# Performance work log

Measured on AMD Instinct MI355X. Metric: run time of the kernel, lower is better.

## Reference

```python
import jax, jax.numpy as jnp
import numpy as np

P = 262144
H = 256
EPS = 1e-12  # torch F.normalize eps


def _l2norm(x):
    # matches torch.nn.functional.normalize(x, dim=-1): x / max(||x||, eps)
    n = jnp.linalg.norm(x, axis=-1, keepdims=True)
    return x / jnp.maximum(n, EPS)


def _mlp(x, params):
    # params: list of (W, b); ReLU on all but last layer
    for W, b in params[:-1]:
        x = jax.nn.relu(x @ W + b)
    W, b = params[-1]
    return x @ W + b


def setup_inputs() -> dict:
    key = jax.random.key(0)
    ks = jax.random.split(key, 24)
    inp = {
        "normals": jax.random.normal(ks[0], (P, 3), dtype=jnp.float32),
        "view_dirs": jax.random.normal(ks[1], (P, 3), dtype=jnp.float32),
        "roughness": jax.random.uniform(ks[2], (P, 1), dtype=jnp.float32),
        "r0": jax.random.uniform(ks[3], (P, 1), dtype=jnp.float32),
    }
    # diffuse MLP: 3 -> 256 -> 256 -> 256 -> 3
    d_dims = [3, H, H, H, 3]
    # specular MLP: 8 -> 256 -> 256 -> 256 -> 3
    s_dims = [8, H, H, H, 3]
    k = 4
    for i in range(4):
        fan = d_dims[i]
        inp[f"dW{i}"] = jax.random.normal(ks[k], (d_dims[i], d_dims[i + 1]), dtype=jnp.float32) * (2.0 / fan) ** 0.5
        inp[f"db{i}"] = jnp.zeros((d_dims[i + 1],), dtype=jnp.float32)
        k += 1
    for i in range(4):
        fan = s_dims[i]
        inp[f"sW{i}"] = jax.random.normal(ks[k], (s_dims[i], s_dims[i + 1]), dtype=jnp.float32) * (2.0 / fan) ** 0.5
        inp[f"sb{i}"] = jnp.zeros((s_dims[i + 1],), dtype=jnp.float32)
        k += 1
    return inp


def reference(normals, view_dirs, roughness, r0,
              dW0, db0, dW1, db1, dW2, db2, dW3, db3,
              sW0, sb0, sW1, sb1, sW2, sb2, sW3, sb3):
    n = _l2norm(normals)
    v = _l2norm(view_dirs)
    inputs_specular = jnp.concatenate((n, v, roughness, r0), axis=-1)  # [P,8]
    visible = (n * v).sum(axis=-1) > 0  # [P]
    d_params = [(dW0, db0), (dW1, db1), (dW2, db2), (dW3, db3)]
    s_params = [(sW0, sb0), (sW1, sb1), (sW2, sb2), (sW3, sb3)]
    # Faithful to gather->MLP->scatter-into-zeros: pointwise MLP computed
    # everywhere, non-visible rows zeroed (identical math, static shapes).
    mask = visible[:, None]
    diffuse_rgb = jnp.where(mask, _mlp(n, d_params), 0.0)
    specular_rgb = jnp.where(mask, _mlp(inputs_specular, s_params), 0.0)
    return (diffuse_rgb, specular_rgb)
```

## Files before the change

kernel.cpp:

```cpp
#include <hip/hip_runtime.h>

typedef _Float16 f16;
typedef _Float16 f16x8 __attribute__((ext_vector_type(8)));
typedef __fp16   fp16x2 __attribute__((ext_vector_type(2)));
typedef float    f32x16 __attribute__((ext_vector_type(16)));
typedef float    f32x4  __attribute__((ext_vector_type(4)));
typedef unsigned int u32;
typedef unsigned int u32x4 __attribute__((ext_vector_type(4)));

#define NPTS 262144

#define NET_F16   143360
#define BIAS_BYTE 573440

static __device__ __forceinline__ u32 pkrtz(float a, float b) {
    fp16x2 h = __builtin_amdgcn_cvt_pkrtz(a, b);
    return __builtin_bit_cast(u32, h);
}
static __device__ __forceinline__ u32 relu_pk(float a, float b) {
    return pkrtz(fmaxf(a, 0.0f), fmaxf(b, 0.0f));
}

__global__ void prep_kernel(
    const float* __restrict__ dW0, const float* __restrict__ db0,
    const float* __restrict__ dW1, const float* __restrict__ db1,
    const float* __restrict__ dW2, const float* __restrict__ db2,
    const float* __restrict__ dW3, const float* __restrict__ db3,
    const float* __restrict__ sW0, const float* __restrict__ sb0,
    const float* __restrict__ sW1, const float* __restrict__ sb1,
    const float* __restrict__ sW2, const float* __restrict__ sb2,
    const float* __restrict__ sW3, const float* __restrict__ sb3,
    f16* __restrict__ wpk, float* __restrict__ bpk)
{
    const int ROWS = 17920;
    int t = blockIdx.x * 256 + threadIdx.x;
    if (t < 2 * ROWS) {
        int net = (t >= ROWS) ? 1 : 0;
        int r = t - net * ROWS;
        const float* W0 = net ? sW0 : dW0;
        const float* W1 = net ? sW1 : dW1;
        const float* W2 = net ? sW2 : dW2;
        const float* W3 = net ? sW3 : dW3;
        int K0 = net ? 8 : 3;
        f16* o = wpk + net * NET_F16;
        if (r < 512) {
            int lane = r & 63;
            int m  = 32 * (r >> 6) + (lane & 31);
            int kb = 8 * (lane >> 5);
            f16* q = o + r * 8;
            #pragma unroll
            for (int j = 0; j < 8; ++j) {
                int k = kb + j;
                q[j] = (f16)((k < K0) ? W0[k * 256 + m] : 0.0f);
            }
        } else if (r < 512 + 8192) {
            int rr = r - 512;
            int lane = rr & 63;
            int hh = lane >> 5;
            int m  = 32 * ((rr >> 6) & 7) + (lane & 31);
            int kt = rr >> 9;
            f16* q = o + 4096 + rr * 8;
            #pragma unroll
            for (int j = 0; j < 8; ++j) {
                int kp = 32 * (kt >> 1) + 16 * (kt & 1) + (j & 3) + 8 * (j >> 2) + 4 * hh;
                q[j] = (f16)W1[kp * 256 + m];
            }
        } else if (r < 512 + 16384) {
            int rr = r - (512 + 8192);
            int lane = rr & 63;
            int hh = lane >> 5;
            int m  = 32 * ((rr >> 6) & 7) + (lane & 31);
            int kt = rr >> 9;
            f16* q = o + 69632 + rr * 8;
            #pragma unroll
            for (int j = 0; j < 8; ++j) {
                int kp = 32 * (kt >> 1) + 16 * (kt & 1) + (j & 3) + 8 * (j >> 2) + 4 * hh;
                q[j] = (f16)W2[kp * 256 + m];
            }
        } else {
            int rr = r - (512 + 16384);
            int lane = rr & 63;
            int hh = lane >> 5;
            int m  = lane & 31;
            int kt = rr >> 6;
            f16* q = o + 135168 + rr * 8;
            #pragma unroll
            for (int j = 0; j < 8; ++j) {
                int kp = 32 * (kt >> 1) + 16 * (kt & 1) + (j & 3) + 8 * (j >> 2) + 4 * hh;
                q[j] = (f16)((m < 3) ? W3[kp * 3 + m] : 0.0f);
            }
        }
    } else if (t < 2 * ROWS + 1600) {
        int tb = t - 2 * ROWS;
        int net = (tb >= 800) ? 1 : 0;
        int i = tb - net * 800;
        float val;
        if (i < 768) {
            int layer = i >> 8;
            const float* bl = net ? (layer == 0 ? sb0 : layer == 1 ? sb1 : sb2)
                                  : (layer == 0 ? db0 : layer == 1 ? db1 : db2);
            int q  = i & 255;
            int rg = q & 15, h = (q >> 4) & 1;
            int m  = 32 * (q >> 5) + (rg & 3) + 8 * (rg >> 2) + 4 * h;
            val = bl[m];
        } else {
            int q  = i - 768;
            int rg = q & 15, h = q >> 4;
            int m  = (rg & 3) + 8 * (rg >> 2) + 4 * h;
            const float* b3 = net ? sb3 : db3;
            val = (m < 3) ? b3[m] : 0.0f;
        }
        bpk[net * 800 + i] = val;
    }
}

#define WAITB(WS) do {                                                          \
    asm volatile("s_waitcnt vmcnt(" WS ") lgkmcnt(0)" ::: "memory");            \
    __builtin_amdgcn_sched_barrier(0);                                          \
    __builtin_amdgcn_s_barrier();                                               \
    __builtin_amdgcn_sched_barrier(0);                                          \
} while (0)

#define STAGE1(S, C0) do {                                                      \
    const u32x4* g_ = ws + (C0) * 512 + woff + lane;                            \
    u32x4* l_ = &ring[S][woff];                                                 \
    __builtin_amdgcn_global_load_lds(                                           \
        (const __attribute__((address_space(1))) void*)g_,                      \
        (__attribute__((address_space(3))) void*)l_, 16, 0, 0);                 \
    __builtin_amdgcn_global_load_lds(                                           \
        (const __attribute__((address_space(1))) void*)(g_ + 64),               \
        (__attribute__((address_space(3))) void*)(l_ + 64), 16, 0, 0);          \
} while (0)
#define STAGE2(S, C0) do {                                                      \
    _Pragma("unroll")                                                           \
    for (int i_ = 0; i_ < 2; ++i_) {                                            \
        const u32x4* g_ = ws + ((C0) + i_) * 512 + woff + lane;                 \
        u32x4* l_ = &ring[S][i_ * 512 + woff];                                  \
        __builtin_amdgcn_global_load_lds(                                       \
            (const __attribute__((address_space(1))) void*)g_,                  \
            (__attribute__((address_space(3))) void*)l_, 16, 0, 0);             \
        __builtin_amdgcn_global_load_lds(                                       \
            (const __attribute__((address_space(1))) void*)(g_ + 64),           \
            (__attribute__((address_space(3))) void*)(l_ + 64), 16, 0, 0);      \
    }                                                                           \
} while (0)

#define CHUNK256(S, CI, KT) do {                                                \
    const u32x4* bq_ = &ring[S][(CI) * 512];                                    \
    const f16x8 xA_ = __builtin_bit_cast(f16x8, xf0[KT]);                       \
    const f16x8 xB_ = __builtin_bit_cast(f16x8, xf1[KT]);                       \
    _Pragma("unroll")                                                           \
    for (int mt_ = 0; mt_ < 8; ++mt_) {                                         \
        const f16x8 a_ = __builtin_bit_cast(f16x8, bq_[mt_ * 64 + lane]);       \
        acc0[mt_] = __builtin_amdgcn_mfma_f32_32x32x16_f16(a_, xA_, acc0[mt_], 0, 0, 0); \
        acc1[mt_] = __builtin_amdgcn_mfma_f32_32x32x16_f16(a_, xB_, acc1[mt_], 0, 0, 0); \
    }                                                                           \
} while (0)

#define BINIT(dst, boff) do {                                                   \
    const f32x4* b4_ = (const f32x4*)(biasl + (boff) + hi * 16);                \
    const f32x4 v0_ = b4_[0], v1_ = b4_[1], v2_ = b4_[2], v3_ = b4_[3];         \
    _Pragma("unroll")                                                           \
    for (int j = 0; j < 4; ++j) {                                               \
        (dst)[j] = v0_[j]; (dst)[4 + j] = v1_[j];                               \
        (dst)[8 + j] = v2_[j]; (dst)[12 + j] = v3_[j];                          \
    }                                                                           \
} while (0)

#define EPI1(ACC, XF) do {                                                      \
    _Pragma("unroll")                                                           \
    for (int mt = 0; mt < 8; ++mt) {                                            \
        _Pragma("unroll")                                                       \
        for (int q = 0; q < 2; ++q) {                                           \
            u32x4 w;                                                            \
            w[0] = relu_pk(ACC[mt][8*q+0], ACC[mt][8*q+1]);                     \
            w[1] = relu_pk(ACC[mt][8*q+2], ACC[mt][8*q+3]);                     \
            w[2] = relu_pk(ACC[mt][8*q+4], ACC[mt][8*q+5]);                     \
            w[3] = relu_pk(ACC[mt][8*q+6], ACC[mt][8*q+7]);                     \
            XF[2*mt+q] = w;                                                     \
        }                                                                       \
    }                                                                           \
} while (0)
#define EPI() do { EPI1(acc0, xf0); EPI1(acc1, xf1); } while (0)

__launch_bounds__(256, 1)
__global__ void mlp_kernel(const float* __restrict__ gn, const float* __restrict__ gv,
                           const float* __restrict__ gro, const float* __restrict__ gr0,
                           const f16* __restrict__ wpk, const float* __restrict__ bpk,
                           float* __restrict__ out)
{
    __shared__ u32x4 ring[3][1024];
    __shared__ __align__(16) float biasl[1600];

    const int tid  = threadIdx.x;
    const int wv   = tid >> 6;
    const int lane = tid & 63;
    const int l32  = lane & 31;
    const int hi   = lane >> 5;
    const int pA   = blockIdx.x * 256 + wv * 64 + l32;
    const int pB   = pA + 32;
    const int woff = wv * 128;
    const u32x4* ws = (const u32x4*)wpk;

    biasl[tid]        = bpk[tid];
    biasl[tid + 256]  = bpk[tid + 256];
    biasl[tid + 512]  = bpk[tid + 512];
    biasl[tid + 768]  = bpk[tid + 768];
    biasl[tid + 1024] = bpk[tid + 1024];
    biasl[tid + 1280] = bpk[tid + 1280];
    if (tid < 64) biasl[tid + 1536] = bpk[tid + 1536];

    STAGE1(0, 0);
    STAGE2(1, 1);

    u32x4 xdA = {0,0,0,0}, xsA = {0,0,0,0}, xdB = {0,0,0,0}, xsB = {0,0,0,0};
    bool visA = false, visB = false;
    if (hi == 0) {
        {
            float nx = gn[3*pA], ny = gn[3*pA+1], nz = gn[3*pA+2];
            float vx = gv[3*pA], vy = gv[3*pA+1], vz = gv[3*pA+2];
            float ro = gro[pA], rr = gr0[pA];
            float ni = 1.0f / fmaxf(sqrtf(nx*nx + ny*ny + nz*nz), 1e-12f);
            float vi = 1.0f / fmaxf(sqrtf(vx*vx + vy*vy + vz*vz), 1e-12f);
            nx *= ni; ny *= ni; nz *= ni; vx *= vi; vy *= vi; vz *= vi;
            visA = (nx*vx + ny*vy + nz*vz) > 0.0f;
            xdA[0] = pkrtz(nx, ny); xdA[1] = pkrtz(nz, 0.0f);
            xsA[0] = xdA[0];        xsA[1] = pkrtz(nz, vx);
            xsA[2] = pkrtz(vy, vz); xsA[3] = pkrtz(ro, rr);
        }
        {
            float nx = gn[3*pB], ny = gn[3*pB+1], nz = gn[3*pB+2];
            float vx = gv[3*pB], vy = gv[3*pB+1], vz = gv[3*pB+2];
            float ro = gro[pB], rr = gr0[pB];
            float ni = 1.0f / fmaxf(sqrtf(nx*nx + ny*ny + nz*nz), 1e-12f);
            float vi = 1.0f / fmaxf(sqrtf(vx*vx + vy*vy + vz*vz), 1e-12f);
            nx *= ni; ny *= ni; nz *= ni; vx *= vi; vy *= vi; vz *= vi;
            visB = (nx*vx + ny*vy + nz*vz) > 0.0f;
            xdB[0] = pkrtz(nx, ny); xdB[1] = pkrtz(nz, 0.0f);
            xsB[0] = xdB[0];        xsB[1] = pkrtz(nz, vx);
            xsB[2] = pkrtz(vy, vz); xsB[3] = pkrtz(ro, rr);
        }
    }

    f32x16 acc0[8], acc1[8];
    u32x4  xf0[16], xf1[16];

    #pragma unroll
    for (int net = 0; net < 2; ++net) {
        const int cb = net * 35;
        const int bb = net * 800;
        const f16x8 xhA = __builtin_bit_cast(f16x8, net ? xsA : xdA);
        const f16x8 xhB = __builtin_bit_cast(f16x8, net ? xsB : xdB);

        WAITB("4");
        STAGE2(2, cb + 3);
        {
            const u32x4* bufq = &ring[0][0];
            #pragma unroll
            for (int mt = 0; mt < 8; ++mt) {
                f32x16 ci;
                BINIT(ci, bb + mt * 32);
                const f16x8 a = __builtin_bit_cast(f16x8, bufq[mt * 64 + lane]);
                acc0[mt] = __builtin_amdgcn_mfma_f32_32x32x16_f16(a, xhA, ci, 0, 0, 0);
                acc1[mt] = __builtin_amdgcn_mfma_f32_32x32x16_f16(a, xhB, ci, 0, 0, 0);
            }
        }
        EPI();

        #pragma unroll
        for (int mt = 0; mt < 8; ++mt) { BINIT(acc0[mt], bb + 256 + mt * 32); BINIT(acc1[mt], bb + 256 + mt * 32); }
        #pragma unroll
        for (int t = 1; t <= 8; ++t) {
            WAITB("4");
            STAGE2((t + 2) % 3, cb + 2 * t + 3);
            CHUNK256(t % 3, 0, 2 * t - 2);
            CHUNK256(t % 3, 1, 2 * t - 1);
        }
        EPI();

        #pragma unroll
        for (int mt = 0; mt < 8; ++mt) { BINIT(acc0[mt], bb + 512 + mt * 32); BINIT(acc1[mt], bb + 512 + mt * 32); }
        #pragma unroll
        for (int t = 9; t <= 15; ++t) {
            WAITB("4");
            STAGE2((t + 2) % 3, cb + 2 * t + 3);
            CHUNK256(t % 3, 0, 2 * t - 18);
            CHUNK256(t % 3, 1, 2 * t - 17);
        }
        WAITB("4");
        if (net == 0) STAGE1(0, 35);
        CHUNK256(16 % 3, 0, 14);
        CHUNK256(16 % 3, 1, 15);
        EPI();

        if (net == 0) { WAITB("2"); STAGE2(1, 36); }
        else          { WAITB("0"); }
        {
            f32x16 c30, c31;
            BINIT(c30, bb + 768);
            BINIT(c31, bb + 768);
            const u32x4* bq0 = &ring[2][0];
            const u32x4* bq1 = &ring[2][512];
            #pragma unroll
            for (int i = 0; i < 8; ++i) {
                const f16x8 a = __builtin_bit_cast(f16x8, bq0[i * 64 + lane]);
                c30 = __builtin_amdgcn_mfma_f32_32x32x16_f16(a, __builtin_bit_cast(f16x8, xf0[i]), c30, 0, 0, 0);
                c31 = __builtin_amdgcn_mfma_f32_32x32x16_f16(a, __builtin_bit_cast(f16x8, xf1[i]), c31, 0, 0, 0);
            }
            #pragma unroll
            for (int i = 0; i < 8; ++i) {
                const f16x8 a = __builtin_bit_cast(f16x8, bq1[i * 64 + lane]);
                c30 = __builtin_amdgcn_mfma_f32_32x32x16_f16(a, __builtin_bit_cast(f16x8, xf0[8 + i]), c30, 0, 0, 0);
                c31 = __builtin_amdgcn_mfma_f32_32x32x16_f16(a, __builtin_bit_cast(f16x8, xf1[8 + i]), c31, 0, 0, 0);
            }
            if (hi == 0) {
                float* opA = out + net * (NPTS * 3) + pA * 3;
                float* opB = out + net * (NPTS * 3) + pB * 3;
                opA[0] = visA ? c30[0] : 0.0f;
                opA[1] = visA ? c30[1] : 0.0f;
                opA[2] = visA ? c30[2] : 0.0f;
                opB[0] = visB ? c31[0] : 0.0f;
                opB[1] = visB ? c31[1] : 0.0f;
                opB[2] = visB ? c31[2] : 0.0f;
            }
        }
    }
}

extern "C" void kernel_launch(void* const* d_in, const int* in_sizes, int n_in,
                              void* d_out, int out_size, void* d_ws, size_t ws_size,
                              hipStream_t stream)
{
    f16*   wpk = (f16*)d_ws;
    float* bpk = (float*)((char*)d_ws + BIAS_BYTE);

    prep_kernel<<<147, 256, 0, stream>>>(
        (const float*)d_in[4],  (const float*)d_in[5],
        (const float*)d_in[6],  (const float*)d_in[7],
        (const float*)d_in[8],  (const float*)d_in[9],
        (const float*)d_in[10], (const float*)d_in[11],
        (const float*)d_in[12], (const float*)d_in[13],
        (const float*)d_in[14], (const float*)d_in[15],
        (const float*)d_in[16], (const float*)d_in[17],
        (const float*)d_in[18], (const float*)d_in[19],
        wpk, bpk);

    mlp_kernel<<<1024, 256, 0, stream>>>(
        (const float*)d_in[0], (const float*)d_in[1],
        (const float*)d_in[2], (const float*)d_in[3],
        wpk, bpk, (float*)d_out);
}
```

Measured before the change: 158.1 us.

## Halve points per wave to fit two blocks per CU

Each wave now processes one 32-point MFMA column tile instead of two, which halves the accumulator and activation register footprint. Launch bounds are raised to two blocks per CU and the grid is doubled, to gain latency hiding across blocks. In exchange, each weight fragment read from LDS feeds one MFMA instead of two, and total weight traffic from global memory doubles. A barrier is also added after the input normalisation.

```diff
diff --git a/kernel.cpp b/kernel.cpp
--- a/kernel.cpp
+++ b/kernel.cpp
@@ -147,13 +147,11 @@
 
 #define CHUNK256(S, CI, KT) do {                                                \
     const u32x4* bq_ = &ring[S][(CI) * 512];                                    \
-    const f16x8 xA_ = __builtin_bit_cast(f16x8, xf0[KT]);                       \
-    const f16x8 xB_ = __builtin_bit_cast(f16x8, xf1[KT]);                       \
+    const f16x8 xh_ = __builtin_bit_cast(f16x8, xf[KT]);                        \
     _Pragma("unroll")                                                           \
     for (int mt_ = 0; mt_ < 8; ++mt_) {                                         \
         const f16x8 a_ = __builtin_bit_cast(f16x8, bq_[mt_ * 64 + lane]);       \
-        acc0[mt_] = __builtin_amdgcn_mfma_f32_32x32x16_f16(a_, xA_, acc0[mt_], 0, 0, 0); \
-        acc1[mt_] = __builtin_amdgcn_mfma_f32_32x32x16_f16(a_, xB_, acc1[mt_], 0, 0, 0); \
+        acc[mt_] = __builtin_amdgcn_mfma_f32_32x32x16_f16(a_, xh_, acc[mt_], 0, 0, 0); \
     }                                                                           \
 } while (0)
 
@@ -167,23 +165,22 @@
     }                                                                           \
 } while (0)
 
-#define EPI1(ACC, XF) do {                                                      \
+#define EPI() do {                                                              \
     _Pragma("unroll")                                                           \
     for (int mt = 0; mt < 8; ++mt) {                                            \
         _Pragma("unroll")                                                       \
         for (int q = 0; q < 2; ++q) {                                           \
             u32x4 w;                                                            \
-            w[0] = relu_pk(ACC[mt][8*q+0], ACC[mt][8*q+1]);                     \
-            w[1] = relu_pk(ACC[mt][8*q+2], ACC[mt][8*q+3]);                     \
-            w[2] = relu_pk(ACC[mt][8*q+4], ACC[mt][8*q+5]);                     \
-            w[3] = relu_pk(ACC[mt][8*q+6], ACC[mt][8*q+7]);                     \
-            XF[2*mt+q] = w;                                                     \
+            w[0] = relu_pk(acc[mt][8*q+0], acc[mt][8*q+1]);                     \
+            w[1] = relu_pk(acc[mt][8*q+2], acc[mt][8*q+3]);                     \
+            w[2] = relu_pk(acc[mt][8*q+4], acc[mt][8*q+5]);                     \
+            w[3] = relu_pk(acc[mt][8*q+6], acc[mt][8*q+7]);                     \
+            xf[2*mt+q] = w;                                                     \
         }                                                                       \
     }                                                                           \
 } while (0)
-#define EPI() do { EPI1(acc0, xf0); EPI1(acc1, xf1); } while (0)
-
-__launch_bounds__(256, 1)
+
+__launch_bounds__(256, 2)
 __global__ void mlp_kernel(const float* __restrict__ gn, const float* __restrict__ gv,
                            const float* __restrict__ gro, const float* __restrict__ gr0,
                            const f16* __restrict__ wpk, const float* __restrict__ bpk,
@@ -197,8 +194,7 @@
     const int lane = tid & 63;
     const int l32  = lane & 31;
     const int hi   = lane >> 5;
-    const int pA   = blockIdx.x * 256 + wv * 64 + l32;
-    const int pB   = pA + 32;
+    const int p    = blockIdx.x * 128 + wv * 32 + l32;
     const int woff = wv * 128;
     const u32x4* ws = (const u32x4*)wpk;
 
@@ -210,47 +206,34 @@
     biasl[tid + 1280] = bpk[tid + 1280];
     if (tid < 64) biasl[tid + 1536] = bpk[tid + 1536];
 
+    u32x4 xd = {0,0,0,0}, xs = {0,0,0,0};
+    bool vis = false;
+    if (hi == 0) {
+        float nx = gn[3*p], ny = gn[3*p+1], nz = gn[3*p+2];
+        float vx = gv[3*p], vy = gv[3*p+1], vz = gv[3*p+2];
+        float ro = gro[p], rr = gr0[p];
+        float ni = 1.0f / fmaxf(sqrtf(nx*nx + ny*ny + nz*nz), 1e-12f);
+        float vi = 1.0f / fmaxf(sqrtf(vx*vx + vy*vy + vz*vz), 1e-12f);
+        nx *= ni; ny *= ni; nz *= ni; vx *= vi; vy *= vi; vz *= vi;
+        vis = (nx*vx + ny*vy + nz*vz) > 0.0f;
+        xd[0] = pkrtz(nx, ny); xd[1] = pkrtz(nz, 0.0f);
+        xs[0] = xd[0];         xs[1] = pkrtz(nz, vx);
+        xs[2] = pkrtz(vy, vz); xs[3] = pkrtz(ro, rr);
+    }
+
+    __syncthreads();
+
     STAGE1(0, 0);
     STAGE2(1, 1);
 
-    u32x4 xdA = {0,0,0,0}, xsA = {0,0,0,0}, xdB = {0,0,0,0}, xsB = {0,0,0,0};
-    bool visA = false, visB = false;
-    if (hi == 0) {
-        {
-            float nx = gn[3*pA], ny = gn[3*pA+1], nz = gn[3*pA+2];
-            float vx = gv[3*pA], vy = gv[3*pA+1], vz = gv[3*pA+2];
-            float ro = gro[pA], rr = gr0[pA];
-            float ni = 1.0f / fmaxf(sqrtf(nx*nx + ny*ny + nz*nz), 1e-12f);
-            float vi = 1.0f / fmaxf(sqrtf(vx*vx + vy*vy + vz*vz), 1e-12f);
-            nx *= ni; ny *= ni; nz *= ni; vx *= vi; vy *= vi; vz *= vi;
-            visA = (nx*vx + ny*vy + nz*vz) > 0.0f;
-            xdA[0] = pkrtz(nx, ny); xdA[1] = pkrtz(nz, 0.0f);
-            xsA[0] = xdA[0];        xsA[1] = pkrtz(nz, vx);
-            xsA[2] = pkrtz(vy, vz); xsA[3] = pkrtz(ro, rr);
-        }
-        {
-            float nx = gn[3*pB], ny = gn[3*pB+1], nz = gn[3*pB+2];
-            float vx = gv[3*pB], vy = gv[3*pB+1], vz = gv[3*pB+2];
-            float ro = gro[pB], rr = gr0[pB];
-            float ni = 1.0f / fmaxf(sqrtf(nx*nx + ny*ny + nz*nz), 1e-12f);
-            float vi = 1.0f / fmaxf(sqrtf(vx*vx + vy*vy + vz*vz), 1e-12f);
-            nx *= ni; ny *= ni; nz *= ni; vx *= vi; vy *= vi; vz *= vi;
-            visB = (nx*vx + ny*vy + nz*vz) > 0.0f;
-            xdB[0] = pkrtz(nx, ny); xdB[1] = pkrtz(nz, 0.0f);
-            xsB[0] = xdB[0];        xsB[1] = pkrtz(nz, vx);
-            xsB[2] = pkrtz(vy, vz); xsB[3] = pkrtz(ro, rr);
-        }
-    }
-
-    f32x16 acc0[8], acc1[8];
-    u32x4  xf0[16], xf1[16];
+    f32x16 acc[8];
+    u32x4  xf[16];
 
     #pragma unroll
     for (int net = 0; net < 2; ++net) {
         const int cb = net * 35;
         const int bb = net * 800;
-        const f16x8 xhA = __builtin_bit_cast(f16x8, net ? xsA : xdA);
-        const f16x8 xhB = __builtin_bit_cast(f16x8, net ? xsB : xdB);
+        const f16x8 xh0 = __builtin_bit_cast(f16x8, net ? xs : xd);
 
         WAITB("4");
         STAGE2(2, cb + 3);
@@ -261,14 +244,13 @@
                 f32x16 ci;
                 BINIT(ci, bb + mt * 32);
                 const f16x8 a = __builtin_bit_cast(f16x8, bufq[mt * 64 + lane]);
-                acc0[mt] = __builtin_amdgcn_mfma_f32_32x32x16_f16(a, xhA, ci, 0, 0, 0);
-                acc1[mt] = __builtin_amdgcn_mfma_f32_32x32x16_f16(a, xhB, ci, 0, 0, 0);
+                acc[mt] = __builtin_amdgcn_mfma_f32_32x32x16_f16(a, xh0, ci, 0, 0, 0);
             }
         }
         EPI();
 
         #pragma unroll
-        for (int mt = 0; mt < 8; ++mt) { BINIT(acc0[mt], bb + 256 + mt * 32); BINIT(acc1[mt], bb + 256 + mt * 32); }
+        for (int mt = 0; mt < 8; ++mt) BINIT(acc[mt], bb + 256 + mt * 32);
         #pragma unroll
         for (int t = 1; t <= 8; ++t) {
             WAITB("4");
@@ -279,7 +261,7 @@
         EPI();
 
         #pragma unroll
-        for (int mt = 0; mt < 8; ++mt) { BINIT(acc0[mt], bb + 512 + mt * 32); BINIT(acc1[mt], bb + 512 + mt * 32); }
+        for (int mt = 0; mt < 8; ++mt) BINIT(acc[mt], bb + 512 + mt * 32);
         #pragma unroll
         for (int t = 9; t <= 15; ++t) {
             WAITB("4");
@@ -296,32 +278,25 @@
         if (net == 0) { WAITB("2"); STAGE2(1, 36); }
         else          { WAITB("0"); }
         {
-            f32x16 c30, c31;
-            BINIT(c30, bb + 768);
-            BINIT(c31, bb + 768);
+            f32x16 c3;
+            BINIT(c3, bb + 768);
             const u32x4* bq0 = &ring[2][0];
             const u32x4* bq1 = &ring[2][512];
             #pragma unroll
             for (int i = 0; i < 8; ++i) {
                 const f16x8 a = __builtin_bit_cast(f16x8, bq0[i * 64 + lane]);
-                c30 = __builtin_amdgcn_mfma_f32_32x32x16_f16(a, __builtin_bit_cast(f16x8, xf0[i]), c30, 0, 0, 0);
-                c31 = __builtin_amdgcn_mfma_f32_32x32x16_f16(a, __builtin_bit_cast(f16x8, xf1[i]), c31, 0, 0, 0);
+                c3 = __builtin_amdgcn_mfma_f32_32x32x16_f16(a, __builtin_bit_cast(f16x8, xf[i]), c3, 0, 0, 0);
             }
             #pragma unroll
             for (int i = 0; i < 8; ++i) {
                 const f16x8 a = __builtin_bit_cast(f16x8, bq1[i * 64 + lane]);
-                c30 = __builtin_amdgcn_mfma_f32_32x32x16_f16(a, __builtin_bit_cast(f16x8, xf0[8 + i]), c30, 0, 0, 0);
-                c31 = __builtin_amdgcn_mfma_f32_32x32x16_f16(a, __builtin_bit_cast(f16x8, xf1[8 + i]), c31, 0, 0, 0);
+                c3 = __builtin_amdgcn_mfma_f32_32x32x16_f16(a, __builtin_bit_cast(f16x8, xf[8 + i]), c3, 0, 0, 0);
             }
             if (hi == 0) {
-                float* opA = out + net * (NPTS * 3) + pA * 3;
-                float* opB = out + net * (NPTS * 3) + pB * 3;
-                opA[0] = visA ? c30[0] : 0.0f;
-                opA[1] = visA ? c30[1] : 0.0f;
-                opA[2] = visA ? c30[2] : 0.0f;
-                opB[0] = visB ? c31[0] : 0.0f;
-                opB[1] = visB ? c31[1] : 0.0f;
-                opB[2] = visB ? c31[2] : 0.0f;
+                float* op = out + net * (NPTS * 3) + p * 3;
+                op[0] = vis ? c3[0] : 0.0f;
+                op[1] = vis ? c3[1] : 0.0f;
+                op[2] = vis ? c3[2] : 0.0f;
             }
         }
     }
@@ -345,7 +320,7 @@
         (const float*)d_in[18], (const float*)d_in[19],
         wpk, bpk);
 
-    mlp_kernel<<<1024, 256, 0, stream>>>(
+    mlp_kernel<<<2048, 256, 0, stream>>>(
         (const float*)d_in[0], (const float*)d_in[1],
         (const float*)d_in[2], (const float*)d_in[3],
         wpk, bpk, (float*)d_out);
```

Result: faster. 149.0 us (-5.7%).
